# Kernel optimization log

Measured on AMD Instinct MI355X. Metric: run time of the kernel, lower is better.

The kernel has to match this reference:

```python
import jax, jax.numpy as jnp
import numpy as np

N, M, D, DV = 8192, 8192, 128, 128

def setup_inputs() -> dict:
    key = jax.random.key(0)
    kq, kk, kv = jax.random.split(key, 3)
    return {
        "Q": jax.random.normal(kq, (N, D), dtype=jnp.float32),
        "K": jax.random.normal(kk, (M, D), dtype=jnp.float32),
        "V": jax.random.normal(kv, (M, DV), dtype=jnp.float32),
    }

def reference(Q, K, V):
    # scores: [N, M] = Q @ K^T (no 1/sqrt(d) scaling, matching the source)
    scores = jnp.einsum("nd,md->nm", Q, K)
    attention_weights = jax.nn.softmax(scores, axis=1)  # softmax over keys
    return jnp.einsum("nm,mv->nv", attention_weights, V)  # [N, DV]
```

## Files before the change

### kernel.cpp

```cpp
#include <hip/hip_runtime.h>
#include <hip/hip_bf16.h>

#define NQ   8192
#define NKEY 8192
#define DH   128

#define BQ   128
#define BK   64
#define BUFB 32768
#define LOG2E 1.44269504088896340736f

typedef __attribute__((ext_vector_type(8)))  short    short8;
typedef __attribute__((ext_vector_type(4)))  short    short4v;
typedef _Float16 half8 __attribute__((ext_vector_type(8)));
typedef __attribute__((ext_vector_type(16))) float    f32x16;
typedef __attribute__((ext_vector_type(4)))  float    float4v;

union BFU { __hip_bfloat16 b; unsigned short u; };
__device__ __forceinline__ unsigned short f2bf(float x) { BFU u; u.b = __float2bfloat16(x); return u.u; }

__device__ __forceinline__ void full_drain_barrier() {
    __builtin_amdgcn_s_waitcnt(0);
    __syncthreads();
}

__global__ void prep(const float* __restrict__ K, const float* __restrict__ V,
                     _Float16* __restrict__ Kh, unsigned short* __restrict__ Vt) {
    __shared__ __attribute__((aligned(16))) unsigned short tile[64 * 72];
    int b = blockIdx.x;
    int t = threadIdx.x;
    if (b < 512) {
        int idx = (b * 256 + t) * 8;
        float4v x0 = *(const float4v*)(K + idx);
        float4v x1 = *(const float4v*)(K + idx + 4);
        half8 o;
#pragma unroll
        for (int j = 0; j < 4; ++j) { o[j] = (_Float16)x0[j]; o[4 + j] = (_Float16)x1[j]; }
        *(half8*)(Kh + idx) = o;
    } else {
        int tv = b - 512;
        int m0 = (tv >> 1) * 64, n0 = (tv & 1) * 64;
#pragma unroll
        for (int it = 0; it < 4; ++it) {
            int id = t + it * 256;
            int mm = id >> 4, nn0 = (id & 15) * 4;
            int mmP = (mm & ~12) | ((mm & 4) << 1) | ((mm & 8) >> 1);
            float4v x = *(const float4v*)(V + (size_t)(m0 + mm) * DH + n0 + nn0);
#pragma unroll
            for (int j = 0; j < 4; ++j)
                tile[(nn0 + j) * 72 + mmP] = f2bf(x[j]);
        }
        __syncthreads();
        int nn = t >> 2, ch = t & 3;
        *(short8*)(Vt + (size_t)(n0 + nn) * NKEY + m0 + ch * 16)     = *(const short8*)&tile[nn * 72 + ch * 16];
        *(short8*)(Vt + (size_t)(n0 + nn) * NKEY + m0 + ch * 16 + 8) = *(const short8*)&tile[nn * 72 + ch * 16 + 8];
    }
}

__launch_bounds__(256, 2)
__global__ void attn_fwd(const float* __restrict__ Q,
                         const _Float16* __restrict__ Kh,
                         const unsigned short* __restrict__ Vt,
                         unsigned short* __restrict__ Opart, float* __restrict__ lpart,
                         float* __restrict__ out, int KS) {
    __shared__ __attribute__((aligned(16))) unsigned short sbuf[2 * BUFB / 2];

    const int tid  = threadIdx.x;
    const int lane = tid & 63;
    const int w    = tid >> 6;
    const int l31  = lane & 31;
    const int h    = lane >> 5;

    const int s  = blockIdx.x % KS;
    const int qb = blockIdx.x / KS;
    const int mlen   = NKEY / KS;
    const int kbase  = s * mlen;
    const int ntiles = mlen / BK;

    const char* gbase[8]; int mult[8]; int ldsoff[8];
#pragma unroll
    for (int i = 0; i < 8; ++i) {
        int Lb = w * 512 + i * 64;
        int L  = Lb + lane;
        const char* gb; int mu;
        if (Lb < 1024) { int r = L >> 4, cg = (L & 15) ^ (r & 15);
                         gb = (const char*)Kh + r * 256 + cg * 16; mu = 256; }
        else           { int Lv = L - 1024; int n = Lv >> 3, cg = (Lv & 7) ^ (n & 7);
                         gb = (const char*)Vt + (size_t)n * (NKEY * 2) + cg * 16; mu = 2; }
        gbase[i] = gb; mult[i] = mu; ldsoff[i] = Lb * 16;
    }

    const int qrow = qb * BQ + w * 32 + l31;
    half8 qf[8];
#pragma unroll
    for (int c = 0; c < 8; ++c) {
        const float* qp = Q + (size_t)qrow * DH + c * 16 + h * 8;
        float4v x0 = *(const float4v*)qp;
        float4v x1 = *(const float4v*)(qp + 4);
#pragma unroll
        for (int i = 0; i < 4; ++i) {
            qf[c][i]     = (_Float16)(x0[i] * LOG2E);
            qf[c][4 + i] = (_Float16)(x1[i] * LOG2E);
        }
    }

    int koff[8];
#pragma unroll
    for (int c = 0; c < 8; ++c)
        koff[c] = l31 * 256 + (((c * 2 + h) ^ (l31 & 15)) << 4);
    int voff[4];
#pragma unroll
    for (int c2 = 0; c2 < 4; ++c2)
        voff[c2] = 16384 + l31 * 128 + (((c2 * 2 + h) ^ (l31 & 7)) << 4);

    float lsum = 0.0f;
    f32x16 O[4];
#pragma unroll
    for (int ct = 0; ct < 4; ++ct)
#pragma unroll
        for (int r = 0; r < 16; ++r) O[ct][r] = 0.0f;

    auto stage = [&](int t, int bufbyte) {
        int kb = kbase + t * BK;
#pragma unroll
        for (int i = 0; i < 8; ++i) {
            const char* g = gbase[i] + (size_t)kb * mult[i];
            __builtin_amdgcn_global_load_lds(
                (const __attribute__((address_space(1))) unsigned int*)g,
                (__attribute__((address_space(3))) unsigned int*)((char*)sbuf + bufbyte + ldsoff[i]),
                16, 0, 0);
        }
    };

    auto compute_tile = [&](int BUF) {
        const char* bp = (const char*)sbuf + BUF;
        f32x16 S0, S1;
#pragma unroll
        for (int r = 0; r < 16; ++r) { S0[r] = 0.0f; S1[r] = 0.0f; }
#pragma unroll
        for (int c = 0; c < 8; ++c) {
            half8 k0 = *(const half8*)(bp + koff[c]);
            half8 k1 = *(const half8*)(bp + koff[c] + 8192);
            S0 = __builtin_amdgcn_mfma_f32_32x32x16_f16(k0, qf[c], S0, 0, 0, 0);
            S1 = __builtin_amdgcn_mfma_f32_32x32x16_f16(k1, qf[c], S1, 0, 0, 0);
        }
        float p0[16], p1[16]; float ps = 0.0f;
#pragma unroll
        for (int r = 0; r < 16; ++r) { p0[r] = __builtin_amdgcn_exp2f(S0[r]); ps += p0[r]; }
#pragma unroll
        for (int r = 0; r < 16; ++r) { p1[r] = __builtin_amdgcn_exp2f(S1[r]); ps += p1[r]; }
        ps += __shfl_xor(ps, 32, 64);
        lsum += ps;
        union PU { unsigned int u[4]; short8 s8; } B[4];
#pragma unroll
        for (int j = 0; j < 4; ++j) {
            B[0].u[j] = __builtin_amdgcn_perm(__float_as_uint(p0[2*j+1]), __float_as_uint(p0[2*j]),   0x07060302u);
            B[1].u[j] = __builtin_amdgcn_perm(__float_as_uint(p0[2*j+9]), __float_as_uint(p0[2*j+8]), 0x07060302u);
            B[2].u[j] = __builtin_amdgcn_perm(__float_as_uint(p1[2*j+1]), __float_as_uint(p1[2*j]),   0x07060302u);
            B[3].u[j] = __builtin_amdgcn_perm(__float_as_uint(p1[2*j+9]), __float_as_uint(p1[2*j+8]), 0x07060302u);
        }
#pragma unroll
        for (int ct = 0; ct < 4; ++ct) {
#pragma unroll
            for (int c2 = 0; c2 < 4; ++c2) {
                short8 va = *(const short8*)(bp + voff[c2] + ct * 4096);
                O[ct] = __builtin_amdgcn_mfma_f32_32x32x16_bf16(va, B[c2].s8, O[ct], 0, 0, 0);
            }
        }
    };

    stage(0, 0);
    for (int t = 0; t < ntiles; t += 2) {
        full_drain_barrier();
        stage(t + 1, BUFB);
        compute_tile(0);
        full_drain_barrier();
        if (t + 2 < ntiles) stage(t + 2, 0);
        compute_tile(BUFB);
    }

    {
        unsigned short* Ob = Opart + ((size_t)s * NQ + qrow) * DH;
#pragma unroll
        for (int ct = 0; ct < 4; ++ct)
#pragma unroll
            for (int g = 0; g < 4; ++g) {
                short4v v;
#pragma unroll
                for (int j = 0; j < 4; ++j) v[j] = (short)f2bf(O[ct][4 * g + j]);
                *(short4v*)(Ob + ct * 32 + 8 * g + 4 * h) = v;
            }
        if (h == 0)
            lpart[(size_t)s * NQ + qrow] = lsum;
    }
}

__global__ void attn_combine(const unsigned short* __restrict__ Opart,
                             const float* __restrict__ lpart, float* __restrict__ out, int KS) {
    int idx = blockIdx.x * 256 + threadIdx.x;
    int row = idx >> 5;
    int col = (idx & 31) << 2;
    float den = 0.0f;
    float a0 = 0.0f, a1 = 0.0f, a2 = 0.0f, a3 = 0.0f;
    for (int s2 = 0; s2 < KS; ++s2) {
        den += lpart[(size_t)s2 * NQ + row];
        const unsigned short* op = Opart + ((size_t)s2 * NQ + row) * DH + col;
        uint2 u = *(const uint2*)op;
        a0 += __uint_as_float(u.x << 16);
        a1 += __uint_as_float(u.x & 0xffff0000u);
        a2 += __uint_as_float(u.y << 16);
        a3 += __uint_as_float(u.y & 0xffff0000u);
    }
    float r = 1.0f / den;
    float4v v; v[0] = a0 * r; v[1] = a1 * r; v[2] = a2 * r; v[3] = a3 * r;
    *(float4v*)(out + (size_t)row * DH + col) = v;
}

extern "C" void kernel_launch(void* const* d_in, const int* in_sizes, int n_in,
                              void* d_out, int out_size, void* d_ws, size_t ws_size,
                              hipStream_t stream) {
    const float* Q = (const float*)d_in[0];
    const float* K = (const float*)d_in[1];
    const float* V = (const float*)d_in[2];
    float* out = (float*)d_out;

    const size_t prep_bytes = 2 * (size_t)NKEY * DH * sizeof(unsigned short);
    int KS = 8;
    while (KS > 1 &&
           ws_size < prep_bytes + (size_t)KS * ((size_t)NQ * DH * 2 + NQ * 4))
        KS >>= 1;

    _Float16* Kh = (_Float16*)d_ws;
    unsigned short* Vt = (unsigned short*)(Kh + (size_t)NKEY * DH);
    unsigned short* Opart = Vt + (size_t)NKEY * DH;
    float* lpart = (float*)(Opart + (size_t)KS * NQ * DH);

    hipLaunchKernelGGL(prep, dim3(768), dim3(256), 0, stream, K, V, Kh, Vt);
    hipLaunchKernelGGL(attn_fwd, dim3((NQ / BQ) * KS), dim3(256), 0, stream,
                       Q, Kh, Vt, Opart, lpart, out, KS);
    hipLaunchKernelGGL(attn_combine, dim3((NQ * DH) / 4 / 256), dim3(256), 0, stream,
                       Opart, lpart, out, KS);
}
```

Before: 114.1 us.

## Software-pipeline QK of next tile with PV of current tile using triple-buffered K

Halves the key tile to 32, keeps K in three LDS buffers and V in two, and restructures the loop so the QK^T MFMAs for tile t+1 are issued alongside the exp and PV MFMAs for tile t. The goal is to overlap the softmax exponentials with matrix work and to hide load latency behind a deeper prefetch. The cost is one drain barrier per 32-key tile instead of one per 64, extra live registers for the carried score tile, and a new V swizzle pattern.

```diff
diff --git a/kernel.cpp b/kernel.cpp
--- a/kernel.cpp
+++ b/kernel.cpp
@@ -6,8 +6,12 @@
 #define DH   128
 
 #define BQ   128
-#define BK   64
-#define BUFB 32768
+#define BK   32
+#define KB0 0
+#define KB1 8192
+#define KB2 16384
+#define VB0 24576
+#define VB1 32768
 #define LOG2E 1.44269504088896340736f
 
 typedef __attribute__((ext_vector_type(8)))  short    short8;
@@ -63,7 +67,7 @@
                          const unsigned short* __restrict__ Vt,
                          unsigned short* __restrict__ Opart, float* __restrict__ lpart,
                          float* __restrict__ out, int KS) {
-    __shared__ __attribute__((aligned(16))) unsigned short sbuf[2 * BUFB / 2];
+    __shared__ __attribute__((aligned(16))) char sbuf[40960];
 
     const int tid  = threadIdx.x;
     const int lane = tid & 63;
@@ -77,17 +81,16 @@
     const int kbase  = s * mlen;
     const int ntiles = mlen / BK;
 
-    const char* gbase[8]; int mult[8]; int ldsoff[8];
-#pragma unroll
-    for (int i = 0; i < 8; ++i) {
-        int Lb = w * 512 + i * 64;
-        int L  = Lb + lane;
-        const char* gb; int mu;
-        if (Lb < 1024) { int r = L >> 4, cg = (L & 15) ^ (r & 15);
-                         gb = (const char*)Kh + r * 256 + cg * 16; mu = 256; }
-        else           { int Lv = L - 1024; int n = Lv >> 3, cg = (Lv & 7) ^ (n & 7);
-                         gb = (const char*)Vt + (size_t)n * (NKEY * 2) + cg * 16; mu = 2; }
-        gbase[i] = gb; mult[i] = mu; ldsoff[i] = Lb * 16;
+    int kgl[2], vgl[2], kld[2], vld[2];
+#pragma unroll
+    for (int i = 0; i < 2; ++i) {
+        int L = w * 128 + i * 64 + lane;
+        int r = L >> 4, ck = (L & 15) ^ (r & 15);
+        kgl[i] = r * 256 + ck * 16;
+        kld[i] = (w * 128 + i * 64) * 16;
+        int n = L >> 2, cv = (L & 3) ^ (n & 3) ^ ((n >> 2) & 3);
+        vgl[i] = n * (NKEY * 2) + cv * 16;
+        vld[i] = (w * 128 + i * 64) * 16;
     }
 
     const int qrow = qb * BQ + w * 32 + l31;
@@ -108,10 +111,10 @@
 #pragma unroll
     for (int c = 0; c < 8; ++c)
         koff[c] = l31 * 256 + (((c * 2 + h) ^ (l31 & 15)) << 4);
-    int voff[4];
-#pragma unroll
-    for (int c2 = 0; c2 < 4; ++c2)
-        voff[c2] = 16384 + l31 * 128 + (((c2 * 2 + h) ^ (l31 & 7)) << 4);
+    int vsw[2];
+#pragma unroll
+    for (int kg = 0; kg < 2; ++kg)
+        vsw[kg] = l31 * 64 + (((kg * 2 + h) ^ (l31 & 3) ^ ((l31 >> 2) & 3)) << 4);
 
     float lsum = 0.0f;
     f32x16 O[4];
@@ -120,63 +123,81 @@
 #pragma unroll
         for (int r = 0; r < 16; ++r) O[ct][r] = 0.0f;
 
-    auto stage = [&](int t, int bufbyte) {
+    auto stageK = [&](int t, int buf) {
         int kb = kbase + t * BK;
-#pragma unroll
-        for (int i = 0; i < 8; ++i) {
-            const char* g = gbase[i] + (size_t)kb * mult[i];
+        const char* g = (const char*)Kh + (size_t)kb * 256;
+#pragma unroll
+        for (int i = 0; i < 2; ++i)
             __builtin_amdgcn_global_load_lds(
-                (const __attribute__((address_space(1))) unsigned int*)g,
-                (__attribute__((address_space(3))) unsigned int*)((char*)sbuf + bufbyte + ldsoff[i]),
+                (const __attribute__((address_space(1))) unsigned int*)(g + kgl[i]),
+                (__attribute__((address_space(3))) unsigned int*)(sbuf + buf + kld[i]),
                 16, 0, 0);
-        }
     };
-
-    auto compute_tile = [&](int BUF) {
-        const char* bp = (const char*)sbuf + BUF;
-        f32x16 S0, S1;
-#pragma unroll
-        for (int r = 0; r < 16; ++r) { S0[r] = 0.0f; S1[r] = 0.0f; }
+    auto stageV = [&](int t, int buf) {
+        int kb = kbase + t * BK;
+        const char* g = (const char*)Vt + (size_t)kb * 2;
+#pragma unroll
+        for (int i = 0; i < 2; ++i)
+            __builtin_amdgcn_global_load_lds(
+                (const __attribute__((address_space(1))) unsigned int*)(g + vgl[i]),
+                (__attribute__((address_space(3))) unsigned int*)(sbuf + buf + vld[i]),
+                16, 0, 0);
+    };
+    auto qk = [&](int buf) -> f32x16 {
+        const char* bp = sbuf + buf;
+        f32x16 S;
+#pragma unroll
+        for (int r = 0; r < 16; ++r) S[r] = 0.0f;
 #pragma unroll
         for (int c = 0; c < 8; ++c) {
-            half8 k0 = *(const half8*)(bp + koff[c]);
-            half8 k1 = *(const half8*)(bp + koff[c] + 8192);
-            S0 = __builtin_amdgcn_mfma_f32_32x32x16_f16(k0, qf[c], S0, 0, 0, 0);
-            S1 = __builtin_amdgcn_mfma_f32_32x32x16_f16(k1, qf[c], S1, 0, 0, 0);
-        }
-        float p0[16], p1[16]; float ps = 0.0f;
-#pragma unroll
-        for (int r = 0; r < 16; ++r) { p0[r] = __builtin_amdgcn_exp2f(S0[r]); ps += p0[r]; }
-#pragma unroll
-        for (int r = 0; r < 16; ++r) { p1[r] = __builtin_amdgcn_exp2f(S1[r]); ps += p1[r]; }
+            half8 kf = *(const half8*)(bp + koff[c]);
+            S = __builtin_amdgcn_mfma_f32_32x32x16_f16(kf, qf[c], S, 0, 0, 0);
+        }
+        return S;
+    };
+
+    stageK(0, KB0);
+    stageK(1, KB1);
+    stageV(0, VB0);
+    full_drain_barrier();
+    f32x16 S = qk(KB0);
+
+    int kRead = KB1, kStage = KB2, kOld = KB0;
+    int vCur = VB0, vNxt = VB1;
+
+    for (int t = 0; t < ntiles; ++t) {
+        if (t + 2 < ntiles) stageK(t + 2, kStage);
+        if (t + 1 < ntiles) stageV(t + 1, vNxt);
+
+        float p[16]; float ps = 0.0f;
+#pragma unroll
+        for (int r = 0; r < 16; ++r) { p[r] = __builtin_amdgcn_exp2f(S[r]); ps += p[r]; }
         ps += __shfl_xor(ps, 32, 64);
         lsum += ps;
-        union PU { unsigned int u[4]; short8 s8; } B[4];
+        union PU { unsigned int u[4]; short8 s8; } B[2];
 #pragma unroll
         for (int j = 0; j < 4; ++j) {
-            B[0].u[j] = __builtin_amdgcn_perm(__float_as_uint(p0[2*j+1]), __float_as_uint(p0[2*j]),   0x07060302u);
-            B[1].u[j] = __builtin_amdgcn_perm(__float_as_uint(p0[2*j+9]), __float_as_uint(p0[2*j+8]), 0x07060302u);
-            B[2].u[j] = __builtin_amdgcn_perm(__float_as_uint(p1[2*j+1]), __float_as_uint(p1[2*j]),   0x07060302u);
-            B[3].u[j] = __builtin_amdgcn_perm(__float_as_uint(p1[2*j+9]), __float_as_uint(p1[2*j+8]), 0x07060302u);
-        }
+            B[0].u[j] = __builtin_amdgcn_perm(__float_as_uint(p[2*j+1]), __float_as_uint(p[2*j]),   0x07060302u);
+            B[1].u[j] = __builtin_amdgcn_perm(__float_as_uint(p[2*j+9]), __float_as_uint(p[2*j+8]), 0x07060302u);
+        }
+
+        f32x16 Snew = S;
+        if (t + 1 < ntiles) Snew = qk(kRead);
+
+        const char* vp = sbuf + vCur;
 #pragma unroll
         for (int ct = 0; ct < 4; ++ct) {
 #pragma unroll
-            for (int c2 = 0; c2 < 4; ++c2) {
-                short8 va = *(const short8*)(bp + voff[c2] + ct * 4096);
-                O[ct] = __builtin_amdgcn_mfma_f32_32x32x16_bf16(va, B[c2].s8, O[ct], 0, 0, 0);
+            for (int kg = 0; kg < 2; ++kg) {
+                short8 va = *(const short8*)(vp + ct * 2048 + vsw[kg]);
+                O[ct] = __builtin_amdgcn_mfma_f32_32x32x16_bf16(va, B[kg].s8, O[ct], 0, 0, 0);
             }
         }
-    };
-
-    stage(0, 0);
-    for (int t = 0; t < ntiles; t += 2) {
+
         full_drain_barrier();
-        stage(t + 1, BUFB);
-        compute_tile(0);
-        full_drain_barrier();
-        if (t + 2 < ntiles) stage(t + 2, 0);
-        compute_tile(BUFB);
+        S = Snew;
+        int tmp = kOld; kOld = kRead; kRead = kStage; kStage = tmp;
+        int tv = vCur; vCur = vNxt; vNxt = tv;
     }
 
     {
```

Result: slower. 118.3 us (+3.7%).

## Software-pipeline QK of next tile with softmax-PV of current tile using split K/V buffers

Applied to the files above, without the earlier changes.

Splits the shared-memory staging into separate double-buffered K and V regions and restructures the main loop so the QK^T MFMAs for tile t+1 are issued alongside the exp/PV work for tile t. K is prefetched two tiles ahead while V is loaded one tile ahead. The aim is to overlap matrix-core work with the exp and permute stalls and with load latency. In exchange it holds two score accumulators live, which raises register pressure under launch_bounds(256,2), and it adds a prologue drain barrier.

```diff
diff --git a/kernel.cpp b/kernel.cpp
--- a/kernel.cpp
+++ b/kernel.cpp
@@ -7,7 +7,10 @@
 
 #define BQ   128
 #define BK   64
-#define BUFB 32768
+#define KBUF0 0
+#define KBUF1 16384
+#define VBUF0 32768
+#define VBUF1 49152
 #define LOG2E 1.44269504088896340736f
 
 typedef __attribute__((ext_vector_type(8)))  short    short8;
@@ -63,7 +66,7 @@
                          const unsigned short* __restrict__ Vt,
                          unsigned short* __restrict__ Opart, float* __restrict__ lpart,
                          float* __restrict__ out, int KS) {
-    __shared__ __attribute__((aligned(16))) unsigned short sbuf[2 * BUFB / 2];
+    __shared__ __attribute__((aligned(16))) char sbuf[65536];
 
     const int tid  = threadIdx.x;
     const int lane = tid & 63;
@@ -77,17 +80,16 @@
     const int kbase  = s * mlen;
     const int ntiles = mlen / BK;
 
-    const char* gbase[8]; int mult[8]; int ldsoff[8];
-#pragma unroll
-    for (int i = 0; i < 8; ++i) {
-        int Lb = w * 512 + i * 64;
+    const char* kgb[4]; int kld[4];
+    const char* vgb[4]; int vld[4];
+#pragma unroll
+    for (int i = 0; i < 4; ++i) {
+        int Lb = w * 256 + i * 64;
         int L  = Lb + lane;
-        const char* gb; int mu;
-        if (Lb < 1024) { int r = L >> 4, cg = (L & 15) ^ (r & 15);
-                         gb = (const char*)Kh + r * 256 + cg * 16; mu = 256; }
-        else           { int Lv = L - 1024; int n = Lv >> 3, cg = (Lv & 7) ^ (n & 7);
-                         gb = (const char*)Vt + (size_t)n * (NKEY * 2) + cg * 16; mu = 2; }
-        gbase[i] = gb; mult[i] = mu; ldsoff[i] = Lb * 16;
+        { int r = L >> 4, ck = (L & 15) ^ (r & 15);
+          kgb[i] = (const char*)Kh + r * 256 + ck * 16; kld[i] = Lb * 16; }
+        { int n = L >> 3, cg = (L & 7) ^ (n & 7);
+          vgb[i] = (const char*)Vt + (size_t)n * (NKEY * 2) + cg * 16; vld[i] = Lb * 16; }
     }
 
     const int qrow = qb * BQ + w * 32 + l31;
@@ -111,7 +113,7 @@
     int voff[4];
 #pragma unroll
     for (int c2 = 0; c2 < 4; ++c2)
-        voff[c2] = 16384 + l31 * 128 + (((c2 * 2 + h) ^ (l31 & 7)) << 4);
+        voff[c2] = l31 * 128 + (((c2 * 2 + h) ^ (l31 & 7)) << 4);
 
     float lsum = 0.0f;
     f32x16 O[4];
@@ -120,21 +122,27 @@
 #pragma unroll
         for (int r = 0; r < 16; ++r) O[ct][r] = 0.0f;
 
-    auto stage = [&](int t, int bufbyte) {
-        int kb = kbase + t * BK;
-#pragma unroll
-        for (int i = 0; i < 8; ++i) {
-            const char* g = gbase[i] + (size_t)kb * mult[i];
+    auto stageK = [&](int t, int buf) {
+        const char* g0 = (const char*)((size_t)(kbase + t * BK) * 256);
+#pragma unroll
+        for (int i = 0; i < 4; ++i)
             __builtin_amdgcn_global_load_lds(
-                (const __attribute__((address_space(1))) unsigned int*)g,
-                (__attribute__((address_space(3))) unsigned int*)((char*)sbuf + bufbyte + ldsoff[i]),
+                (const __attribute__((address_space(1))) unsigned int*)(kgb[i] + (size_t)g0),
+                (__attribute__((address_space(3))) unsigned int*)(sbuf + buf + kld[i]),
                 16, 0, 0);
-        }
-    };
-
-    auto compute_tile = [&](int BUF) {
-        const char* bp = (const char*)sbuf + BUF;
-        f32x16 S0, S1;
+    };
+    auto stageV = [&](int t, int buf) {
+        size_t g0 = (size_t)(kbase + t * BK) * 2;
+#pragma unroll
+        for (int i = 0; i < 4; ++i)
+            __builtin_amdgcn_global_load_lds(
+                (const __attribute__((address_space(1))) unsigned int*)(vgb[i] + g0),
+                (__attribute__((address_space(3))) unsigned int*)(sbuf + buf + vld[i]),
+                16, 0, 0);
+    };
+
+    auto qk64 = [&](int buf, f32x16& S0, f32x16& S1) {
+        const char* bp = sbuf + buf;
 #pragma unroll
         for (int r = 0; r < 16; ++r) { S0[r] = 0.0f; S1[r] = 0.0f; }
 #pragma unroll
@@ -144,6 +152,9 @@
             S0 = __builtin_amdgcn_mfma_f32_32x32x16_f16(k0, qf[c], S0, 0, 0, 0);
             S1 = __builtin_amdgcn_mfma_f32_32x32x16_f16(k1, qf[c], S1, 0, 0, 0);
         }
+    };
+
+    auto sfpv = [&](const f32x16& S0, const f32x16& S1, int vbuf) {
         float p0[16], p1[16]; float ps = 0.0f;
 #pragma unroll
         for (int r = 0; r < 16; ++r) { p0[r] = __builtin_amdgcn_exp2f(S0[r]); ps += p0[r]; }
@@ -159,24 +170,36 @@
             B[2].u[j] = __builtin_amdgcn_perm(__float_as_uint(p1[2*j+1]), __float_as_uint(p1[2*j]),   0x07060302u);
             B[3].u[j] = __builtin_amdgcn_perm(__float_as_uint(p1[2*j+9]), __float_as_uint(p1[2*j+8]), 0x07060302u);
         }
+        const char* vp = sbuf + vbuf;
 #pragma unroll
         for (int ct = 0; ct < 4; ++ct) {
 #pragma unroll
             for (int c2 = 0; c2 < 4; ++c2) {
-                short8 va = *(const short8*)(bp + voff[c2] + ct * 4096);
+                short8 va = *(const short8*)(vp + voff[c2] + ct * 4096);
                 O[ct] = __builtin_amdgcn_mfma_f32_32x32x16_bf16(va, B[c2].s8, O[ct], 0, 0, 0);
             }
         }
     };
 
-    stage(0, 0);
+    f32x16 Sa0, Sa1, Sb0, Sb1;
+    stageK(0, KBUF0);
+    stageK(1, KBUF1);
+    stageV(0, VBUF0);
+    full_drain_barrier();
+    qk64(KBUF0, Sa0, Sa1);
+
     for (int t = 0; t < ntiles; t += 2) {
         full_drain_barrier();
-        stage(t + 1, BUFB);
-        compute_tile(0);
+        if (t + 2 < ntiles) stageK(t + 2, KBUF0);
+        if (t + 1 < ntiles) stageV(t + 1, VBUF1);
+        if (t + 1 < ntiles) qk64(KBUF1, Sb0, Sb1);
+        sfpv(Sa0, Sa1, VBUF0);
+
         full_drain_barrier();
-        if (t + 2 < ntiles) stage(t + 2, 0);
-        compute_tile(BUFB);
+        if (t + 3 < ntiles) stageK(t + 3, KBUF1);
+        if (t + 2 < ntiles) stageV(t + 2, VBUF0);
+        if (t + 2 < ntiles) qk64(KBUF0, Sa0, Sa1);
+        if (t + 1 < ntiles) sfpv(Sb0, Sb1, VBUF1);
     }
 
     {
```

Result: no change. 116.2 us (+1.8%).
